# Kernel tuning notes

Measured on AMD Instinct MI355X. Metric: run time of the kernel, lower is better.

## Reference

```python
import jax, jax.numpy as jnp
import numpy as np

B, S = 64, 512
NQ, RAW, D, H, K = 10000, 256, 256, 64, 4  # vocab, raw emb, model emb, gru state, num_stages
LN_EPS = 1e-5


def setup_inputs() -> dict:
    key = jax.random.key(0)
    ks = jax.random.split(key, 30)
    def n(i, shape, s=0.02):
        return (jax.random.normal(ks[i], shape) * s).astype(jnp.float32)
    return {
        "q": jax.random.randint(ks[0], (B, S), 0, NQ, dtype=jnp.int32),
        "r": jax.random.randint(ks[1], (B, S), 0, 2, dtype=jnp.int32),
        # flattened 4-stage embedding table [NQ*4, RAW]
        "emb_table": n(2, (NQ * K, RAW)),
        # per-stage expert MLPs (weights stored as [in, out])
        "expert_w1": n(3, (K, RAW, RAW)), "expert_b1": n(4, (K, RAW)),
        "expert_w2": n(5, (K, RAW, D)),  "expert_b2": n(6, (K, D)),
        # router input adapter Linear(RAW*4 -> D)
        "adapter_w": n(7, (RAW * K, D)), "adapter_b": n(8, (D,)),
        # interaction reducer Linear(2D -> H)
        "reducer_w": n(9, (2 * D, H)), "reducer_b": n(10, (H,)),
        "start_token": jnp.zeros((1, 1, H), jnp.float32),
        # torch GRU params: [3H, in], gate order (r, z, n)
        "gru_w_ih": n(11, (3 * H, H)), "gru_w_hh": n(12, (3 * H, H)),
        "gru_b_ih": n(13, (3 * H,)),   "gru_b_hh": n(14, (3 * H,)),
        # gate Linear(D+H -> 4)
        "wgate_w": n(15, (D + H, K)), "wgate_b": n(16, (K,)),
        "ln_gamma": jnp.ones((D,), jnp.float32), "ln_beta": jnp.zeros((D,), jnp.float32),
        "resp_table": n(17, (2, D)),
        "proj_cor_w": n(18, (D, D)), "proj_cor_b": n(19, (D,)),
        "proj_inc_w": n(20, (D, D)), "proj_inc_b": n(21, (D,)),
    }


def _forward(q, r, emb_table, expert_w1, expert_b1, expert_w2, expert_b2,
             adapter_w, adapter_b, reducer_w, reducer_b, start_token,
             gru_w_ih, gru_w_hh, gru_b_ih, gru_b_hh, wgate_w, wgate_b,
             ln_gamma, ln_beta, resp_table, proj_cor_w, proj_cor_b,
             proj_inc_w, proj_inc_b):
    b, s = q.shape
    # 4-stage embedding lookup: indices q*4 + [0..3]
    stage_idx = q[..., None] * K + jnp.arange(K)          # [B,S,4]
    q_raw = emb_table[stage_idx]                          # [B,S,4,RAW]
    # smart summary (router input adapter), eval mode -> no dropout
    q_flat = q_raw.reshape(b, s, K * RAW)
    q_summary = jax.nn.relu(q_flat @ adapter_w + adapter_b)  # [B,S,D]
    r_emb = resp_table[r]                                    # [B,S,D]
    gru_in = jnp.concatenate([q_summary, r_emb], -1) @ reducer_w + reducer_b  # [B,S,H]
    start = jnp.broadcast_to(start_token, (b, 1, H))
    x = jnp.concatenate([start, gru_in[:, :-1]], axis=1)     # shifted [B,S,H]
    # GRU over time (torch gate order r,z,n)
    xg = x @ gru_w_ih.T + gru_b_ih                           # [B,S,3H]
    def step(h, xg_t):
        hg = h @ gru_w_hh.T + gru_b_hh
        xr, xz, xn = jnp.split(xg_t, 3, axis=-1)
        hr, hz, hn = jnp.split(hg, 3, axis=-1)
        rg = jax.nn.sigmoid(xr + hr)
        zg = jax.nn.sigmoid(xz + hz)
        ng = jnp.tanh(xn + rg * hn)
        h_new = (1.0 - zg) * ng + zg * h
        return h_new, h_new
    _, m = jax.lax.scan(step, jnp.zeros((b, H), x.dtype), xg.transpose(1, 0, 2))
    m_seq = m.transpose(1, 0, 2)                             # [B,S,H]
    # parallel experts (vectorized over the 4 stages)
    h1 = jax.nn.relu(jnp.einsum('bske,keh->bskh', q_raw, expert_w1) + expert_b1)
    experts = jnp.einsum('bskh,khd->bskd', h1, expert_w2) + expert_b2  # [B,S,4,D]
    # noisy routing (eval: no noise), top-1 mask, softmax gating
    logits = jnp.concatenate([q_summary, m_seq], -1) @ wgate_w + wgate_b  # [B,S,4]
    gate_probs = jax.nn.softmax(logits, axis=-1)
    top1 = jnp.argmax(logits, axis=-1)
    onehot = jax.nn.one_hot(top1, K, dtype=logits.dtype)
    masked = jnp.where(onehot > 0, logits, -jnp.inf)
    gate_w = jax.nn.softmax(masked, axis=-1)                 # one-hot for top_k=1
    combined = jnp.einsum('bskd,bsk->bsd', experts, gate_w)  # [B,S,D]
    # layer norm
    mu = combined.mean(-1, keepdims=True)
    var = combined.var(-1, keepdims=True)
    q_fused = ln_gamma * (combined - mu) * jax.lax.rsqrt(var + LN_EPS) + ln_beta
    emb_cor = q_fused @ proj_cor_w + proj_cor_b
    emb_inc = q_fused @ proj_inc_w + proj_inc_b
    rm = r[..., None].astype(q_fused.dtype)
    qa_fused = emb_cor * rm + emb_inc * (1.0 - rm)
    return q_fused, qa_fused, gate_probs


def reference(q, r, emb_table, expert_w1, expert_b1, expert_w2, expert_b2,
              adapter_w, adapter_b, reducer_w, reducer_b, start_token,
              gru_w_ih, gru_w_hh, gru_b_ih, gru_b_hh, wgate_w, wgate_b,
              ln_gamma, ln_beta, resp_table, proj_cor_w, proj_cor_b,
              proj_inc_w, proj_inc_b):
    q_fused, qa_fused, _ = _forward(q, r, emb_table, expert_w1, expert_b1,
                                    expert_w2, expert_b2, adapter_w, adapter_b,
                                    reducer_w, reducer_b, start_token,
                                    gru_w_ih, gru_w_hh, gru_b_ih, gru_b_hh,
                                    wgate_w, wgate_b, ln_gamma, ln_beta,
                                    resp_table, proj_cor_w, proj_cor_b,
                                    proj_inc_w, proj_inc_b)
    return (q_fused, qa_fused)
```

## Files before the change

kernel.cpp:

```cpp
#include <hip/hip_runtime.h>
#include <cstddef>


#define NQ 10000
#define TT 32768

typedef __attribute__((ext_vector_type(8))) short bf16x8;
typedef __attribute__((ext_vector_type(4))) float f32x4;

__device__ double g_qs  [NQ * 256];
__device__ double g_xgr [2 * 192];
__device__ float  g_xg0f[192];
__device__ float  g_xq2 [NQ * 384];
__device__ double g_lq  [NQ * 4];
__device__ float  g_m   [TT * 64];
__device__ int    g_top1[TT];
__device__ unsigned short g_w1t  [4 * 256 * 256];
__device__ unsigned short g_w2t  [4 * 256 * 256];
__device__ unsigned short g_projt[512 * 256];
__device__ unsigned short g_qf   [NQ * 4 * 256];

__device__ __forceinline__ float bf2f(unsigned short x) {
  return __uint_as_float(((unsigned)x) << 16);
}
__device__ __forceinline__ unsigned short f2bf(float f) {
  unsigned u = __float_as_uint(f);
  u += 0x7FFFu + ((u >> 16) & 1u);
  return (unsigned short)(u >> 16);
}
__device__ __forceinline__ f32x4 mfma16(bf16x8 a, bf16x8 b, f32x4 c) {
  return __builtin_amdgcn_mfma_f32_16x16x32_bf16(a, b, c, 0, 0, 0);
}
__device__ __forceinline__ void pkfma(float2& c, float2 a, float2 b) {
  asm("v_pk_fma_f32 %0, %1, %2, %0" : "+v"(c) : "v"(a), "v"(b));
}

__device__ __forceinline__ double fexp(double x) {
  const double L2E  = 1.4426950408889634074;
  const double LN2H = 6.93147180369123816490e-01;
  const double LN2L = 1.90821492927058770002e-10;
  double n = rint(x * L2E);
  int ni = (int)n;
  double r = fma(-n, LN2H, x);
  r = fma(-n, LN2L, r);
  double p = 2.7557319223985888e-07;
  p = fma(p, r, 2.7557319223985893e-06);
  p = fma(p, r, 2.4801587301587302e-05);
  p = fma(p, r, 1.9841269841269841e-04);
  p = fma(p, r, 1.3888888888888889e-03);
  p = fma(p, r, 8.3333333333333332e-03);
  p = fma(p, r, 4.1666666666666664e-02);
  p = fma(p, r, 1.6666666666666666e-01);
  p = fma(p, r, 0.5);
  p = fma(p, r, 1.0);
  p = fma(p, r, 1.0);
  return ldexp(p, ni);
}

__device__ __forceinline__ double tpoly(double p) {
  const double p2 = p * p;
  double t = -1382.0 / 155925.0;
  t = fma(t, p2, 62.0 / 2835.0);
  t = fma(t, p2, -17.0 / 315.0);
  t = fma(t, p2, 2.0 / 15.0);
  t = fma(t, p2, -1.0 / 3.0);
  t = fma(t, p2, 1.0);
  return p * t;
}

__global__ void __launch_bounds__(256) prepqsk_kernel(
    const float* __restrict__ expert_w1, const float* __restrict__ expert_w2,
    const float* __restrict__ proj_cor_w, const float* __restrict__ proj_inc_w,
    const float* __restrict__ resp_table, const float* __restrict__ reducer_w,
    const float* __restrict__ reducer_b,  const float* __restrict__ start_token,
    const float* __restrict__ gru_w_ih,   const float* __restrict__ gru_b_ih,
    const float* __restrict__ emb, const float* __restrict__ adapter_w,
    const float* __restrict__ adapter_b)
{
  __shared__ double red2f[128];
  __shared__ __align__(16) float As[64][33];
  __shared__ __align__(16) float Bs[32][65];
  const int tid = threadIdx.x;

  if (blockIdx.x < 64) {
    if (blockIdx.x == 0) {
      if (tid < 128) {
        const int rr = tid >> 6, j = tid & 63;
        double acc = (double)reducer_b[j];
        for (int k = 0; k < 256; ++k)
          acc += (double)resp_table[rr * 256 + k] *
                 (double)reducer_w[(256 + k) * 64 + j];
        red2f[tid] = acc;
      }
      __syncthreads();
      if (tid < 192) {
        const double bih = (double)gru_b_ih[tid];
        double a0 = bih, a1 = bih, a2 = bih;
        for (int j = 0; j < 64; ++j) {
          const double w = (double)gru_w_ih[tid * 64 + j];
          a0 += red2f[j] * w;
          a1 += red2f[64 + j] * w;
          a2 += (double)start_token[j] * w;
        }
        g_xgr[tid] = a0; g_xgr[192 + tid] = a1; g_xg0f[tid] = (float)a2;
      }
    }
    const int idx0 = blockIdx.x * 256 + tid;
    const int stride = 64 * 256;
    for (int i = idx0; i < 4 * 256 * 256; i += stride) {
      const int e = i >> 16, rem = i & 65535, n = rem >> 8, k = rem & 255;
      g_w1t[i] = f2bf(expert_w1[e * 65536 + k * 256 + n]);
      g_w2t[i] = f2bf(expert_w2[e * 65536 + k * 256 + n]);
    }
    for (int i = idx0; i < 512 * 256; i += stride) {
      const int n = i >> 8, k = i & 255;
      g_projt[i] = f2bf((n < 256) ? proj_cor_w[k * 256 + n]
                                  : proj_inc_w[k * 256 + (n - 256)]);
    }
    return;
  }

  const int bq = blockIdx.x - 64;
  const int q0 = (bq >> 2) * 64;
  const int n0 = (bq & 3) * 64;
  const int ty = tid >> 4, tx = tid & 15;

  double acc[4][4];
#pragma unroll
  for (int i = 0; i < 4; ++i)
#pragma unroll
    for (int j = 0; j < 4; ++j) acc[i][j] = 0.0;

  const int arow = tid >> 2, aks = (tid & 3) * 8;
  const int qa = min(q0 + arow, NQ - 1);
  const int bkk = tid >> 3, bns = (tid & 7) * 8;

  for (int kc = 0; kc < 1024; kc += 32) {
    f32x4 av0 = *(const f32x4*)(emb + (size_t)qa * 1024 + kc + aks);
    f32x4 av1 = *(const f32x4*)(emb + (size_t)qa * 1024 + kc + aks + 4);
    f32x4 bv0 = *(const f32x4*)(adapter_w + (size_t)(kc + bkk) * 256 + n0 + bns);
    f32x4 bv1 = *(const f32x4*)(adapter_w + (size_t)(kc + bkk) * 256 + n0 + bns + 4);
    __syncthreads();
#pragma unroll
    for (int i = 0; i < 4; ++i) { As[arow][aks + i] = av0[i]; As[arow][aks + 4 + i] = av1[i]; }
#pragma unroll
    for (int i = 0; i < 4; ++i) { Bs[bkk][bns + i] = bv0[i]; Bs[bkk][bns + 4 + i] = bv1[i]; }
    __syncthreads();
#pragma unroll 4
    for (int kk = 0; kk < 32; ++kk) {
      double a[4], b[4];
#pragma unroll
      for (int i = 0; i < 4; ++i) a[i] = (double)As[ty * 4 + i][kk];
#pragma unroll
      for (int j = 0; j < 4; ++j) b[j] = (double)Bs[kk][tx * 4 + j];
#pragma unroll
      for (int i = 0; i < 4; ++i)
#pragma unroll
        for (int j = 0; j < 4; ++j) acc[i][j] = fma(a[i], b[j], acc[i][j]);
    }
  }
#pragma unroll
  for (int i = 0; i < 4; ++i) {
    const int qrow = q0 + ty * 4 + i;
    if (qrow < NQ) {
#pragma unroll
      for (int j = 0; j < 4; ++j) {
        const int n = n0 + tx * 4 + j;
        double v = acc[i][j] + (double)adapter_b[n];
        g_qs[(size_t)qrow * 256 + n] = v > 0.0 ? v : 0.0;
      }
    }
  }
}

__global__ void __launch_bounds__(256) smallk_kernel(
    const float* __restrict__ reducer_w, const float* __restrict__ gru_w_ih,
    const float* __restrict__ wgate_w)
{
  __shared__ double qsr[256];
  __shared__ double ps[4][64];
  __shared__ double gi[64];
  const int tid = threadIdx.x;
  const int qq = blockIdx.x;
  qsr[tid] = g_qs[(size_t)qq * 256 + tid];
  __syncthreads();
  {
    const int j = tid & 63, h = tid >> 6;
    const int k0 = h * 64;
    double a0 = 0.0, a1 = 0.0, a2 = 0.0, a3 = 0.0;
    for (int k = 0; k < 64; k += 4) {
      a0 = fma(qsr[k0 + k + 0], (double)reducer_w[(k0 + k + 0) * 64 + j], a0);
      a1 = fma(qsr[k0 + k + 1], (double)reducer_w[(k0 + k + 1) * 64 + j], a1);
      a2 = fma(qsr[k0 + k + 2], (double)reducer_w[(k0 + k + 2) * 64 + j], a2);
      a3 = fma(qsr[k0 + k + 3], (double)reducer_w[(k0 + k + 3) * 64 + j], a3);
    }
    ps[h][j] = (a0 + a1) + (a2 + a3);
  }
  __syncthreads();
  if (tid < 64) gi[tid] = (ps[0][tid] + ps[1][tid]) + (ps[2][tid] + ps[3][tid]);
  if (tid >= 64 && tid < 68) {
    const int e = tid - 64;
    double a0 = 0.0, a1 = 0.0, a2 = 0.0, a3 = 0.0;
    for (int k = 0; k < 256; k += 4) {
      a0 = fma(qsr[k + 0], (double)wgate_w[(k + 0) * 4 + e], a0);
      a1 = fma(qsr[k + 1], (double)wgate_w[(k + 1) * 4 + e], a1);
      a2 = fma(qsr[k + 2], (double)wgate_w[(k + 2) * 4 + e], a2);
      a3 = fma(qsr[k + 3], (double)wgate_w[(k + 3) * 4 + e], a3);
    }
    g_lq[(size_t)qq * 4 + e] = (a0 + a1) + (a2 + a3);
  }
  __syncthreads();
  if (tid < 192) {
    double a0 = 0.0, a1 = 0.0, a2 = 0.0, a3 = 0.0;
    for (int k = 0; k < 64; k += 4) {
      a0 = fma(gi[k + 0], (double)gru_w_ih[tid * 64 + k + 0], a0);
      a1 = fma(gi[k + 1], (double)gru_w_ih[tid * 64 + k + 1], a1);
      a2 = fma(gi[k + 2], (double)gru_w_ih[tid * 64 + k + 2], a2);
      a3 = fma(gi[k + 3], (double)gru_w_ih[tid * 64 + k + 3], a3);
    }
    const double s = (a0 + a1) + (a2 + a3);
    g_xq2[(size_t)qq * 384 + tid]       = (float)(s + g_xgr[tid]);
    g_xq2[(size_t)qq * 384 + 192 + tid] = (float)(s + g_xgr[192 + tid]);
  }
}

__global__ void __attribute__((amdgpu_waves_per_eu(1, 1)))
__launch_bounds__(128, 1) gruE_kernel(
    const int* __restrict__ q, const int* __restrict__ r,
    const float* __restrict__ whh, const float* __restrict__ bhh,
    const float* __restrict__ emb,
    const float* __restrict__ b1, const float* __restrict__ b2,
    const float* __restrict__ lng, const float* __restrict__ lnb)
{
  __shared__ __align__(16) float HF[2][68];
  __shared__ __align__(16) unsigned short QR[32 * 264];
  __shared__ __align__(16) unsigned short H1[32 * 264];
  __shared__ __align__(16) unsigned short EO[32 * 264];
  const int tid = threadIdx.x;

  if (blockIdx.x < 64) {
    const int b = blockIdx.x;
    const int wv = tid >> 6;
    const int l = tid & 63;
    const int p = l >> 1;
    const int half = l & 1;
    const int j = wv * 32 + p;
    const int k0 = half * 32;

    float2 Wr[16], Wz[16], Wn[16];
#pragma unroll
    for (int i = 0; i < 16; ++i) {
      Wr[i] = *(const float2*)(whh + (size_t)(0 * 64 + j) * 64 + k0 + 2 * i);
      Wz[i] = *(const float2*)(whh + (size_t)(1 * 64 + j) * 64 + k0 + 2 * i);
      Wn[i] = *(const float2*)(whh + (size_t)(2 * 64 + j) * 64 + k0 + 2 * i);
    }
#pragma unroll
    for (int i = 0; i < 16; ++i) {
      asm volatile("" : "+v"(Wr[i]));
      asm volatile("" : "+v"(Wz[i]));
      asm volatile("" : "+v"(Wn[i]));
    }
    const double br = (double)bhh[j];
    const double bz = (double)bhh[64 + j];
    const double bn = (double)bhh[128 + j];

    float cx0 = g_xg0f[j], cx1 = g_xg0f[64 + j], cx2 = g_xg0f[128 + j];
    int qA = q[b * 512], rA = r[b * 512];

    const int jpad = j + ((j >> 5) << 2);
    if (tid < 64) {
      const int tp = tid + ((tid >> 5) << 2);
      HF[0][tp] = 0.f;
    }
    double hd = 0.0;
    asm volatile("s_waitcnt lgkmcnt(0)\n\ts_barrier" ::: "memory");

    for (int t = 0; t < 512; ++t) {
      float nx0 = 0.f, nx1 = 0.f, nx2 = 0.f;
      int qB = qA, rB = rA;
      if (t < 511) {
        const size_t base = (size_t)(qA * 2 + rA) * 192 + j;
        nx0 = g_xq2[base];
        nx1 = g_xq2[base + 64];
        nx2 = g_xq2[base + 128];
        const int tk = min(t + 1, 510);
        qB = q[b * 512 + tk];
        rB = r[b * 512 + tk];
      }

      float2 ar = {0.f, 0.f}, az = {0.f, 0.f}, an = {0.f, 0.f};
      {
        const float4* hp = (const float4*)&HF[t & 1][half * 36];
#pragma unroll
        for (int g = 0; g < 8; ++g) {
          const float4 t4 = hp[g];
          const float2 hA = make_float2(t4.x, t4.y);
          const float2 hB = make_float2(t4.z, t4.w);
          pkfma(ar, Wr[2 * g], hA); pkfma(ar, Wr[2 * g + 1], hB);
          pkfma(az, Wz[2 * g], hA); pkfma(az, Wz[2 * g + 1], hB);
          pkfma(an, Wn[2 * g], hA); pkfma(an, Wn[2 * g + 1], hB);
        }
      }
      const float srh = ar.x + ar.y;
      const float szh = az.x + az.y;
      const float snh = an.x + an.y;
      const float sro = __shfl_xor(srh, 1);
      const float szo = __shfl_xor(szh, 1);
      const float sno = __shfl_xor(snh, 1);
      const double hr = br + ((double)srh + (double)sro);
      const double hz = bz + ((double)szh + (double)szo);
      const double hn = bn + ((double)snh + (double)sno);
      const double pr = (double)cx0 + hr, pz = (double)cx1 + hz;
      const double xn = (double)cx2;
      double rg = fma(0.5, tpoly(0.5 * pr), 0.5);
      double zg = fma(0.5, tpoly(0.5 * pz), 0.5);
      double pre = fma(rg, hn, xn);
      double ng = tpoly(pre);
      const bool bad = (fabs(pr) > 0.5) | (fabs(pz) > 0.5) | (fabs(pre) > 0.25);
      if (bad) {
        rg = 1.0 / (1.0 + fexp(-pr));
        zg = 1.0 / (1.0 + fexp(-pz));
        pre = fma(rg, hn, xn);
        ng = 1.0 - 2.0 / (fexp(pre + pre) + 1.0);
      }
      const double hnew = fma(zg, hd - ng, ng);
      hd = hnew;
      const float hnf = (float)hnew;
      if (half == 0) {
        HF[(t & 1) ^ 1][jpad] = hnf;
        g_m[((size_t)b * 512 + t) * 64 + j] = hnf;
      }
      asm volatile("s_waitcnt lgkmcnt(0)\n\ts_barrier" ::: "memory");

      cx0 = nx0; cx1 = nx1; cx2 = nx2;
      qA = qB; rA = rB;
    }
    return;
  }

  const int bx = blockIdx.x - 64;
  const int e  = bx & 3;
  const int t0 = (bx >> 2) * 32;
  const int w = tid >> 6;
  const int lane = tid & 63;
  const int l15 = lane & 15;
  const int quad = lane >> 4;

  for (int c = 0; c < 16; ++c) {
    const int idx = c * 128 + tid;
    const int row = idx >> 6, col4 = idx & 63;
    const int qv = min(t0 + row, NQ - 1);
    f32x4 v = *(const f32x4*)(emb + (size_t)qv * 1024 + e * 256 + col4 * 4);
    unsigned a = ((unsigned)f2bf(v[1]) << 16) | f2bf(v[0]);
    unsigned bb = ((unsigned)f2bf(v[3]) << 16) | f2bf(v[2]);
    *(uint2*)&QR[row * 264 + col4 * 4] = make_uint2(a, bb);
  }
  __syncthreads();

  const f32x4 z4 = {0.f, 0.f, 0.f, 0.f};
  const int n0 = w * 128;

  f32x4 acc[2][8];
#pragma unroll
  for (int a = 0; a < 2; ++a)
#pragma unroll
    for (int bq = 0; bq < 8; ++bq) acc[a][bq] = z4;
#pragma unroll
  for (int ks = 0; ks < 8; ++ks) {
    const int koff = ks * 32 + quad * 8;
    bf16x8 a0 = *(const bf16x8*)&QR[l15 * 264 + koff];
    bf16x8 a1 = *(const bf16x8*)&QR[(16 + l15) * 264 + koff];
#pragma unroll
    for (int nt = 0; nt < 8; ++nt) {
      bf16x8 bbv = *(const bf16x8*)(g_w1t + (size_t)e * 65536 +
                                    (size_t)(n0 + nt * 16 + l15) * 256 + koff);
      acc[0][nt] = mfma16(a0, bbv, acc[0][nt]);
      acc[1][nt] = mfma16(a1, bbv, acc[1][nt]);
    }
  }
#pragma unroll
  for (int nt = 0; nt < 8; ++nt) {
    const int n = n0 + nt * 16 + l15;
    const float b1v = b1[e * 256 + n];
#pragma unroll
    for (int mt = 0; mt < 2; ++mt)
#pragma unroll
      for (int rg = 0; rg < 4; ++rg) {
        const int m = mt * 16 + quad * 4 + rg;
        H1[m * 264 + n] = f2bf(fmaxf(acc[mt][nt][rg] + b1v, 0.f));
      }
  }
  __syncthreads();

  f32x4 acc2[2][8];
#pragma unroll
  for (int a = 0; a < 2; ++a)
#pragma unroll
    for (int bq = 0; bq < 8; ++bq) acc2[a][bq] = z4;
#pragma unroll
  for (int ks = 0; ks < 8; ++ks) {
    const int koff = ks * 32 + quad * 8;
    bf16x8 a0 = *(const bf16x8*)&H1[l15 * 264 + koff];
    bf16x8 a1 = *(const bf16x8*)&H1[(16 + l15) * 264 + koff];
#pragma unroll
    for (int nt = 0; nt < 8; ++nt) {
      bf16x8 bbv = *(const bf16x8*)(g_w2t + (size_t)e * 65536 +
                                    (size_t)(n0 + nt * 16 + l15) * 256 + koff);
      acc2[0][nt] = mfma16(a0, bbv, acc2[0][nt]);
      acc2[1][nt] = mfma16(a1, bbv, acc2[1][nt]);
    }
  }
#pragma unroll
  for (int nt = 0; nt < 8; ++nt) {
    const int n = n0 + nt * 16 + l15;
    const float b2v = b2[e * 256 + n];
#pragma unroll
    for (int mt = 0; mt < 2; ++mt)
#pragma unroll
      for (int rg = 0; rg < 4; ++rg) {
        const int m = mt * 16 + quad * 4 + rg;
        EO[m * 264 + n] = f2bf(acc2[mt][nt][rg] + b2v);
      }
  }
  __syncthreads();

  {
    const int m = tid >> 2;
    const int sub = tid & 3;
    float sx = 0.f, sxx = 0.f;
#pragma unroll
    for (int i = 0; i < 8; ++i) {
      bf16x8 v = *(const bf16x8*)&EO[m * 264 + sub * 64 + i * 8];
#pragma unroll
      for (int c = 0; c < 8; ++c) {
        const float f = bf2f((unsigned short)v[c]);
        sx += f; sxx += f * f;
      }
    }
    sx += __shfl_xor(sx, 1); sxx += __shfl_xor(sxx, 1);
    sx += __shfl_xor(sx, 2); sxx += __shfl_xor(sxx, 2);
    const float mu = sx * (1.f / 256.f);
    const float var = sxx * (1.f / 256.f) - mu * mu;
    const float inv = 1.f / sqrtf(var + 1e-5f);
    if (t0 + m < NQ) {
      const size_t base = ((size_t)(t0 + m) * 4 + e) * 256;
#pragma unroll
      for (int i = 0; i < 8; ++i) {
        const int dbase = sub * 64 + i * 8;
        bf16x8 v = *(const bf16x8*)&EO[m * 264 + dbase];
        bf16x8 ov;
#pragma unroll
        for (int c = 0; c < 8; ++c) {
          const int d = dbase + c;
          const float f = bf2f((unsigned short)v[c]);
          ov[c] = (short)f2bf(lng[d] * (f - mu) * inv + lnb[d]);
        }
        *(bf16x8*)(g_qf + base + dbase) = ov;
      }
    }
  }
}

__global__ void __launch_bounds__(256) top1_kernel(
    const int* __restrict__ q,
    const float* __restrict__ wgate_w, const float* __restrict__ wgate_b)
{
  __shared__ double w2[256];
  const int tid = threadIdx.x;
  w2[tid] = (double)wgate_w[1024 + tid];
  __syncthreads();
  const int t = blockIdx.x * 256 + tid;
  const int qv = q[t];
  double l0 = g_lq[(size_t)qv * 4 + 0] + (double)wgate_b[0];
  double l1 = g_lq[(size_t)qv * 4 + 1] + (double)wgate_b[1];
  double l2 = g_lq[(size_t)qv * 4 + 2] + (double)wgate_b[2];
  double l3 = g_lq[(size_t)qv * 4 + 3] + (double)wgate_b[3];
  const f32x4* mr4 = (const f32x4*)(g_m + (size_t)t * 64);
#pragma unroll 4
  for (int jj = 0; jj < 16; ++jj) {
    const f32x4 mv4 = mr4[jj];
#pragma unroll
    for (int c = 0; c < 4; ++c) {
      const double mv = (double)mv4[c];
      const int k = (jj * 4 + c) * 4;
      l0 = fma(mv, w2[k + 0], l0);
      l1 = fma(mv, w2[k + 1], l1);
      l2 = fma(mv, w2[k + 2], l2);
      l3 = fma(mv, w2[k + 3], l3);
    }
  }
  int bi = 0; double bvv = l0;
  if (l1 > bvv) { bvv = l1; bi = 1; }
  if (l2 > bvv) { bvv = l2; bi = 2; }
  if (l3 > bvv) { bvv = l3; bi = 3; }
  g_top1[t] = bi;
}

__global__ void __launch_bounds__(128) kernelF(
    const int* __restrict__ q, const int* __restrict__ r,
    const float* __restrict__ pcb, const float* __restrict__ pib,
    float* __restrict__ out)
{
  __shared__ __align__(16) unsigned short QF[32 * 264];
  __shared__ int rv_l[32];
  const int tid = threadIdx.x;
  const int t0 = blockIdx.x * 32;
  const int w = tid >> 6;
  const int lane = tid & 63;
  const int l15 = lane & 15;
  const int quad = lane >> 4;
  if (tid < 32) rv_l[tid] = r[t0 + tid];
  __syncthreads();

  {
    const int m = tid >> 2;
    const size_t row = ((size_t)q[t0 + m] * 4 + g_top1[t0 + m]) * 256;
#pragma unroll
    for (int i = 0; i < 8; ++i) {
      const int dbase = (tid & 3) * 64 + i * 8;
      bf16x8 v = *(const bf16x8*)(g_qf + row + dbase);
      *(bf16x8*)&QF[m * 264 + dbase] = v;
      f32x4 f0, f1;
#pragma unroll
      for (int c = 0; c < 4; ++c) f0[c] = bf2f((unsigned short)v[c]);
#pragma unroll
      for (int c = 0; c < 4; ++c) f1[c] = bf2f((unsigned short)v[4 + c]);
      *(f32x4*)(out + (size_t)(t0 + m) * 256 + dbase) = f0;
      *(f32x4*)(out + (size_t)(t0 + m) * 256 + dbase + 4) = f1;
    }
  }
  __syncthreads();

  const f32x4 z4 = {0.f, 0.f, 0.f, 0.f};
  const int n0 = w * 128;
  for (int ph = 0; ph < 2; ++ph) {
    f32x4 acc[2][8];
#pragma unroll
    for (int a = 0; a < 2; ++a)
#pragma unroll
      for (int bq = 0; bq < 8; ++bq) acc[a][bq] = z4;
#pragma unroll
    for (int ks = 0; ks < 8; ++ks) {
      const int koff = ks * 32 + quad * 8;
      bf16x8 a0 = *(const bf16x8*)&QF[l15 * 264 + koff];
      bf16x8 a1 = *(const bf16x8*)&QF[(16 + l15) * 264 + koff];
#pragma unroll
      for (int nt = 0; nt < 8; ++nt) {
        bf16x8 bbv = *(const bf16x8*)(g_projt +
            (size_t)(ph * 256 + n0 + nt * 16 + l15) * 256 + koff);
        acc[0][nt] = mfma16(a0, bbv, acc[0][nt]);
        acc[1][nt] = mfma16(a1, bbv, acc[1][nt]);
      }
    }
    const float* pbb = ph ? pib : pcb;
    const int want = ph ? 0 : 1;
#pragma unroll
    for (int nt = 0; nt < 8; ++nt) {
      const int n = n0 + nt * 16 + l15;
      const float pbv = pbb[n];
#pragma unroll
      for (int mt = 0; mt < 2; ++mt)
#pragma unroll
        for (int rg = 0; rg < 4; ++rg) {
          const int m = mt * 16 + quad * 4 + rg;
          if (rv_l[m] == want)
            out[(size_t)TT * 256 + (size_t)(t0 + m) * 256 + n] =
                acc[mt][nt][rg] + pbv;
        }
    }
  }
}

extern "C" void kernel_launch(void* const* d_in, const int* in_sizes, int n_in,
                              void* d_out, int out_size, void* d_ws, size_t ws_size,
                              hipStream_t stream)
{
  const int*   q   = (const int*)d_in[0];
  const int*   r   = (const int*)d_in[1];
  const float* emb = (const float*)d_in[2];
  const float* ew1 = (const float*)d_in[3];
  const float* eb1 = (const float*)d_in[4];
  const float* ew2 = (const float*)d_in[5];
  const float* eb2 = (const float*)d_in[6];
  const float* aw  = (const float*)d_in[7];
  const float* ab  = (const float*)d_in[8];
  const float* rw  = (const float*)d_in[9];
  const float* rb  = (const float*)d_in[10];
  const float* st  = (const float*)d_in[11];
  const float* wih = (const float*)d_in[12];
  const float* whh = (const float*)d_in[13];
  const float* bih = (const float*)d_in[14];
  const float* bhh = (const float*)d_in[15];
  const float* wgw = (const float*)d_in[16];
  const float* wgb = (const float*)d_in[17];
  const float* lng = (const float*)d_in[18];
  const float* lnb = (const float*)d_in[19];
  const float* resp= (const float*)d_in[20];
  const float* pcw = (const float*)d_in[21];
  const float* pcb = (const float*)d_in[22];
  const float* piw = (const float*)d_in[23];
  const float* pib = (const float*)d_in[24];
  float* out = (float*)d_out;
  (void)bih; (void)in_sizes; (void)n_in; (void)d_ws; (void)ws_size; (void)out_size;

  prepqsk_kernel<<<692, 256, 0, stream>>>(ew1, ew2, pcw, piw, resp, rw, rb, st,
                                          wih, bih, emb, aw, ab);
  smallk_kernel<<<NQ, 256, 0, stream>>>(rw, wih, wgw);
  gruE_kernel<<<64 + 313 * 4, 128, 0, stream>>>(q, r, whh, bhh,
                                                emb, eb1, eb2, lng, lnb);
  top1_kernel<<<128, 256, 0, stream>>>(q, wgw, wgb);
  kernelF<<<1024, 128, 0, stream>>>(q, r, pcb, pib, out);
}
```

Measured before the change: 778.8 us.

## Fuse top1 gating into kernelF, batch smallk with LDS weights, transpose As tile

The separate top1 kernel is removed. Each kernelF block now computes the 4 gate logits with 4 threads per token and picks the argmax through lane shuffles, which drops one launch and the g_top1 round trip. smallk now handles 8 questions per block and stages reducer, GRU input and gate weights in LDS once per block, instead of rereading them from global memory for each of 10000 blocks. The adapter GEMM stores its A tile transposed so the inner loop can read it with vector loads. The new smallk uses about 113 KB of LDS per block, which lowers occupancy to one block per CU.

```diff
diff --git a/kernel.cpp b/kernel.cpp
--- a/kernel.cpp
+++ b/kernel.cpp
@@ -14,7 +14,6 @@
 __device__ float  g_xq2 [NQ * 384];
 __device__ double g_lq  [NQ * 4];
 __device__ float  g_m   [TT * 64];
-__device__ int    g_top1[TT];
 __device__ unsigned short g_w1t  [4 * 256 * 256];
 __device__ unsigned short g_w2t  [4 * 256 * 256];
 __device__ unsigned short g_projt[512 * 256];
@@ -78,7 +77,7 @@
     const float* __restrict__ adapter_b)
 {
   __shared__ double red2f[128];
-  __shared__ __align__(16) float As[64][33];
+  __shared__ __align__(16) float As[32][66];
   __shared__ __align__(16) float Bs[32][65];
   const int tid = threadIdx.x;
 
@@ -142,17 +141,22 @@
     f32x4 bv1 = *(const f32x4*)(adapter_w + (size_t)(kc + bkk) * 256 + n0 + bns + 4);
     __syncthreads();
 #pragma unroll
-    for (int i = 0; i < 4; ++i) { As[arow][aks + i] = av0[i]; As[arow][aks + 4 + i] = av1[i]; }
-#pragma unroll
-    for (int i = 0; i < 4; ++i) { Bs[bkk][bns + i] = bv0[i]; Bs[bkk][bns + 4 + i] = bv1[i]; }
+    for (int i = 0; i < 4; ++i) {
+      As[aks + i][arow] = av0[i];
+      As[aks + 4 + i][arow] = av1[i];
+      Bs[bkk][bns + i] = bv0[i];
+      Bs[bkk][bns + 4 + i] = bv1[i];
+    }
     __syncthreads();
 #pragma unroll 4
     for (int kk = 0; kk < 32; ++kk) {
+      const f32x4 af = *(const f32x4*)&As[kk][ty * 4];
+      const f32x4 bf = *(const f32x4*)&Bs[kk][tx * 4];
       double a[4], b[4];
 #pragma unroll
-      for (int i = 0; i < 4; ++i) a[i] = (double)As[ty * 4 + i][kk];
-#pragma unroll
-      for (int j = 0; j < 4; ++j) b[j] = (double)Bs[kk][tx * 4 + j];
+      for (int i = 0; i < 4; ++i) a[i] = (double)af[i];
+#pragma unroll
+      for (int j = 0; j < 4; ++j) b[j] = (double)bf[j];
 #pragma unroll
       for (int i = 0; i < 4; ++i)
 #pragma unroll
@@ -177,50 +181,61 @@
     const float* __restrict__ reducer_w, const float* __restrict__ gru_w_ih,
     const float* __restrict__ wgate_w)
 {
+  __shared__ float rwl[256 * 64];
+  __shared__ float gwl[192 * 64];
+  __shared__ float wgl[256 * 4];
   __shared__ double qsr[256];
   __shared__ double ps[4][64];
   __shared__ double gi[64];
   const int tid = threadIdx.x;
-  const int qq = blockIdx.x;
-  qsr[tid] = g_qs[(size_t)qq * 256 + tid];
-  __syncthreads();
-  {
-    const int j = tid & 63, h = tid >> 6;
-    const int k0 = h * 64;
-    double a0 = 0.0, a1 = 0.0, a2 = 0.0, a3 = 0.0;
-    for (int k = 0; k < 64; k += 4) {
-      a0 = fma(qsr[k0 + k + 0], (double)reducer_w[(k0 + k + 0) * 64 + j], a0);
-      a1 = fma(qsr[k0 + k + 1], (double)reducer_w[(k0 + k + 1) * 64 + j], a1);
-      a2 = fma(qsr[k0 + k + 2], (double)reducer_w[(k0 + k + 2) * 64 + j], a2);
-      a3 = fma(qsr[k0 + k + 3], (double)reducer_w[(k0 + k + 3) * 64 + j], a3);
-    }
-    ps[h][j] = (a0 + a1) + (a2 + a3);
-  }
-  __syncthreads();
-  if (tid < 64) gi[tid] = (ps[0][tid] + ps[1][tid]) + (ps[2][tid] + ps[3][tid]);
-  if (tid >= 64 && tid < 68) {
-    const int e = tid - 64;
-    double a0 = 0.0, a1 = 0.0, a2 = 0.0, a3 = 0.0;
-    for (int k = 0; k < 256; k += 4) {
-      a0 = fma(qsr[k + 0], (double)wgate_w[(k + 0) * 4 + e], a0);
-      a1 = fma(qsr[k + 1], (double)wgate_w[(k + 1) * 4 + e], a1);
-      a2 = fma(qsr[k + 2], (double)wgate_w[(k + 2) * 4 + e], a2);
-      a3 = fma(qsr[k + 3], (double)wgate_w[(k + 3) * 4 + e], a3);
-    }
-    g_lq[(size_t)qq * 4 + e] = (a0 + a1) + (a2 + a3);
-  }
-  __syncthreads();
-  if (tid < 192) {
-    double a0 = 0.0, a1 = 0.0, a2 = 0.0, a3 = 0.0;
-    for (int k = 0; k < 64; k += 4) {
-      a0 = fma(gi[k + 0], (double)gru_w_ih[tid * 64 + k + 0], a0);
-      a1 = fma(gi[k + 1], (double)gru_w_ih[tid * 64 + k + 1], a1);
-      a2 = fma(gi[k + 2], (double)gru_w_ih[tid * 64 + k + 2], a2);
-      a3 = fma(gi[k + 3], (double)gru_w_ih[tid * 64 + k + 3], a3);
-    }
-    const double s = (a0 + a1) + (a2 + a3);
-    g_xq2[(size_t)qq * 384 + tid]       = (float)(s + g_xgr[tid]);
-    g_xq2[(size_t)qq * 384 + 192 + tid] = (float)(s + g_xgr[192 + tid]);
+
+  for (int i = tid; i < 256 * 64; i += 256) rwl[i] = reducer_w[i];
+  for (int i = tid; i < 192 * 64; i += 256) gwl[i] = gru_w_ih[i];
+  for (int i = tid; i < 256 * 4; i += 256) wgl[i] = wgate_w[i];
+
+  for (int g = 0; g < 8; ++g) {
+    const int qq = blockIdx.x * 8 + g;
+    __syncthreads();
+    qsr[tid] = g_qs[(size_t)qq * 256 + tid];
+    __syncthreads();
+    {
+      const int j = tid & 63, h = tid >> 6;
+      const int k0 = h * 64;
+      double a0 = 0.0, a1 = 0.0, a2 = 0.0, a3 = 0.0;
+      for (int k = 0; k < 64; k += 4) {
+        a0 = fma(qsr[k0 + k + 0], (double)rwl[(k0 + k + 0) * 64 + j], a0);
+        a1 = fma(qsr[k0 + k + 1], (double)rwl[(k0 + k + 1) * 64 + j], a1);
+        a2 = fma(qsr[k0 + k + 2], (double)rwl[(k0 + k + 2) * 64 + j], a2);
+        a3 = fma(qsr[k0 + k + 3], (double)rwl[(k0 + k + 3) * 64 + j], a3);
+      }
+      ps[h][j] = (a0 + a1) + (a2 + a3);
+    }
+    __syncthreads();
+    if (tid < 64) gi[tid] = (ps[0][tid] + ps[1][tid]) + (ps[2][tid] + ps[3][tid]);
+    if (tid >= 64 && tid < 68) {
+      const int e = tid - 64;
+      double a0 = 0.0, a1 = 0.0, a2 = 0.0, a3 = 0.0;
+      for (int k = 0; k < 256; k += 4) {
+        a0 = fma(qsr[k + 0], (double)wgl[(k + 0) * 4 + e], a0);
+        a1 = fma(qsr[k + 1], (double)wgl[(k + 1) * 4 + e], a1);
+        a2 = fma(qsr[k + 2], (double)wgl[(k + 2) * 4 + e], a2);
+        a3 = fma(qsr[k + 3], (double)wgl[(k + 3) * 4 + e], a3);
+      }
+      g_lq[(size_t)qq * 4 + e] = (a0 + a1) + (a2 + a3);
+    }
+    __syncthreads();
+    if (tid < 192) {
+      double a0 = 0.0, a1 = 0.0, a2 = 0.0, a3 = 0.0;
+      for (int k = 0; k < 64; k += 4) {
+        a0 = fma(gi[k + 0], (double)gwl[tid * 64 + k + 0], a0);
+        a1 = fma(gi[k + 1], (double)gwl[tid * 64 + k + 1], a1);
+        a2 = fma(gi[k + 2], (double)gwl[tid * 64 + k + 2], a2);
+        a3 = fma(gi[k + 3], (double)gwl[tid * 64 + k + 3], a3);
+      }
+      const double s = (a0 + a1) + (a2 + a3);
+      g_xq2[(size_t)qq * 384 + tid]       = (float)(s + g_xgr[tid]);
+      g_xq2[(size_t)qq * 384 + 192 + tid] = (float)(s + g_xgr[192 + tid]);
+    }
   }
 }
 
@@ -461,47 +476,14 @@
   }
 }
 
-__global__ void __launch_bounds__(256) top1_kernel(
-    const int* __restrict__ q,
-    const float* __restrict__ wgate_w, const float* __restrict__ wgate_b)
-{
-  __shared__ double w2[256];
-  const int tid = threadIdx.x;
-  w2[tid] = (double)wgate_w[1024 + tid];
-  __syncthreads();
-  const int t = blockIdx.x * 256 + tid;
-  const int qv = q[t];
-  double l0 = g_lq[(size_t)qv * 4 + 0] + (double)wgate_b[0];
-  double l1 = g_lq[(size_t)qv * 4 + 1] + (double)wgate_b[1];
-  double l2 = g_lq[(size_t)qv * 4 + 2] + (double)wgate_b[2];
-  double l3 = g_lq[(size_t)qv * 4 + 3] + (double)wgate_b[3];
-  const f32x4* mr4 = (const f32x4*)(g_m + (size_t)t * 64);
-#pragma unroll 4
-  for (int jj = 0; jj < 16; ++jj) {
-    const f32x4 mv4 = mr4[jj];
-#pragma unroll
-    for (int c = 0; c < 4; ++c) {
-      const double mv = (double)mv4[c];
-      const int k = (jj * 4 + c) * 4;
-      l0 = fma(mv, w2[k + 0], l0);
-      l1 = fma(mv, w2[k + 1], l1);
-      l2 = fma(mv, w2[k + 2], l2);
-      l3 = fma(mv, w2[k + 3], l3);
-    }
-  }
-  int bi = 0; double bvv = l0;
-  if (l1 > bvv) { bvv = l1; bi = 1; }
-  if (l2 > bvv) { bvv = l2; bi = 2; }
-  if (l3 > bvv) { bvv = l3; bi = 3; }
-  g_top1[t] = bi;
-}
-
 __global__ void __launch_bounds__(128) kernelF(
     const int* __restrict__ q, const int* __restrict__ r,
+    const float* __restrict__ wgate_w, const float* __restrict__ wgate_b,
     const float* __restrict__ pcb, const float* __restrict__ pib,
     float* __restrict__ out)
 {
   __shared__ __align__(16) unsigned short QF[32 * 264];
+  __shared__ double w2d[256];
   __shared__ int rv_l[32];
   const int tid = threadIdx.x;
   const int t0 = blockIdx.x * 32;
@@ -510,11 +492,47 @@
   const int l15 = lane & 15;
   const int quad = lane >> 4;
   if (tid < 32) rv_l[tid] = r[t0 + tid];
+  w2d[tid] = (double)wgate_w[1024 + tid];
+  w2d[128 + tid] = (double)wgate_w[1152 + tid];
   __syncthreads();
+
+  int bi;
+  {
+    const int tok = tid >> 2;
+    const int e = tid & 3;
+    const int t = t0 + tok;
+    const int qv = q[t];
+    double le = g_lq[(size_t)qv * 4 + e] + (double)wgate_b[e];
+    const f32x4* mr4 = (const f32x4*)(g_m + (size_t)t * 64);
+#pragma unroll 4
+    for (int jj = 0; jj < 16; ++jj) {
+      const f32x4 mv4 = mr4[jj];
+#pragma unroll
+      for (int c = 0; c < 4; ++c)
+        le = fma((double)mv4[c], w2d[(jj * 4 + c) * 4 + e], le);
+    }
+    double v = le; bi = e;
+    {
+      const double vo = __shfl_xor(v, 1);
+      const int bo = __shfl_xor(bi, 1);
+      const bool ilow = (e & 1) == 0;
+      const double vl = ilow ? v : vo, vh = ilow ? vo : v;
+      const int bl = ilow ? bi : bo, bh = ilow ? bo : bi;
+      if (vh > vl) { v = vh; bi = bh; } else { v = vl; bi = bl; }
+    }
+    {
+      const double vo = __shfl_xor(v, 2);
+      const int bo = __shfl_xor(bi, 2);
+      const bool ilow = (e & 2) == 0;
+      const double vl = ilow ? v : vo, vh = ilow ? vo : v;
+      const int bl = ilow ? bi : bo, bh = ilow ? bo : bi;
+      if (vh > vl) { v = vh; bi = bh; } else { v = vl; bi = bl; }
+    }
+  }
 
   {
     const int m = tid >> 2;
-    const size_t row = ((size_t)q[t0 + m] * 4 + g_top1[t0 + m]) * 256;
+    const size_t row = ((size_t)q[t0 + m] * 4 + bi) * 256;
 #pragma unroll
     for (int i = 0; i < 8; ++i) {
       const int dbase = (tid & 3) * 64 + i * 8;
@@ -605,9 +623,8 @@
 
   prepqsk_kernel<<<692, 256, 0, stream>>>(ew1, ew2, pcw, piw, resp, rw, rb, st,
                                           wih, bih, emb, aw, ab);
-  smallk_kernel<<<NQ, 256, 0, stream>>>(rw, wih, wgw);
+  smallk_kernel<<<1250, 256, 0, stream>>>(rw, wih, wgw);
   gruE_kernel<<<64 + 313 * 4, 128, 0, stream>>>(q, r, whh, bhh,
                                                 emb, eb1, eb2, lng, lnb);
-  top1_kernel<<<128, 256, 0, stream>>>(q, wgw, wgb);
-  kernelF<<<1024, 128, 0, stream>>>(q, r, pcb, pib, out);
-}
+  kernelF<<<1024, 128, 0, stream>>>(q, r, wgw, wgb, pcb, pib, out);
+}
```

Result: slower. 909.1 us (+16.7%).
